# Kernel tuning notes

Hardware: AMD Instinct MI355X
Metric: run time of the kernel (lower is better)

## Reference

```python
import jax, jax.numpy as jnp
import numpy as np

B, C, H, W = 4, 128, 128, 128
_PARAM_IDS = ["1", "2", "4", "5", "7", "8", "9", "10", "12", "13", "15", "16"]


def setup_inputs() -> dict:
    key = jax.random.key(0)
    ks = jax.random.split(key, 2 + 2 * len(_PARAM_IDS))
    scale = 1.0 / np.sqrt(C).astype(np.float32)
    inp = {
        "x": jax.random.normal(ks[0], (B, C, H, W), jnp.float32),
        "y": jax.random.uniform(ks[1], (B, C, H, W), jnp.float32),  # edge gate in [0,1)
    }
    for i, n in enumerate(_PARAM_IDS):
        inp[f"w{n}"] = jax.random.normal(ks[2 + 2 * i], (C, C), jnp.float32) * scale
        inp[f"b{n}"] = jax.random.normal(ks[3 + 2 * i], (C,), jnp.float32) * scale
    return inp


def pw(t, w, b):
    # kernel-size-1 Conv1d: t [B,C,M] -> [B,C,M]
    return jnp.einsum('oc,bcm->bom', w, t) + b[None, :, None]


def gated_scan(seq_x, seq_y, wa, ba, wb, bb, relu_first):
    # seq_x, seq_y: [L, B, C, M]; recurrence h_k = relu(conv_a(x_k) + conv_b(h_{k-1}) * y_{k-1})
    first = jax.nn.relu(seq_x[0]) if relu_first else seq_x[0]

    def step(prev, inp):
        xi, yp = inp
        h = jax.nn.relu(pw(xi, wa, ba) + pw(prev, wb, bb) * yp)
        return h, h

    _, outs = jax.lax.scan(step, first, (seq_x[1:], seq_y[:-1]))
    return jnp.concatenate([first[None], outs], axis=0)


def reference(x, y, w1, b1, w2, b2, w4, b4, w5, b5, w7, b7, w8, b8,
              w9, b9, w10, b10, w12, b12, w13, b13, w15, b15, w16, b16):
    rows_x = jnp.transpose(x, (2, 0, 1, 3))   # [H,B,C,W]
    rows_y = jnp.transpose(y, (2, 0, 1, 3))   # [H,B,C,W]
    y_cols = jnp.transpose(y, (3, 0, 1, 2))   # [W,B,C,H]

    # south scan over height (row 0 untouched, no relu on it)
    hs_rows = gated_scan(rows_x, rows_y, w1, b1, w2, b2, relu_first=False)
    hs_cols = jnp.transpose(hs_rows, (3, 1, 2, 0))  # [W,B,C,H]
    # south-east / south-west scans over width (boundary column gets relu)
    hse = gated_scan(hs_cols, y_cols, w4, b4, w5, b5, relu_first=True)
    hsw = gated_scan(hs_cols[::-1], y_cols[::-1], w7, b7, w8, b8, relu_first=True)[::-1]

    # north scan over height (reversed; boundary row gets relu)
    hn_rows = gated_scan(rows_x[::-1], rows_y[::-1], w9, b9, w10, b10, relu_first=True)[::-1]
    hn_cols = jnp.transpose(hn_rows, (3, 1, 2, 0))  # [W,B,C,H]
    hne = gated_scan(hn_cols, y_cols, w12, b12, w13, b13, relu_first=True)
    hnw = gated_scan(hn_cols[::-1], y_cols[::-1], w15, b15, w16, b16, relu_first=True)[::-1]

    out_cols = hse + hsw + hne + hnw  # [W,B,C,H]
    return jnp.transpose(out_cols, (1, 2, 3, 0))  # [B,C,H,W]
```

## Files before the change

### kernel.cpp

```cpp
#include <hip/hip_runtime.h>

typedef unsigned int uint;
typedef unsigned short ushort;
typedef __attribute__((ext_vector_type(8))) short short8;
typedef __attribute__((ext_vector_type(4))) float f32x4;

#define NPOS 16384
#define PLANE 2097152
#define XR_OFF 0
#define GR_OFF 32768
#define HP_OFF 65536
#define OR_OFF 81920
#define LDS_PH1 81920
#define LDS_PH2 114688

__device__ __forceinline__ uint fbits(float a) { return __builtin_bit_cast(uint, a); }
__device__ __forceinline__ uint rnehi(float a) {
  const uint u = fbits(a);
  return (u + 0x7FFFu + ((u >> 16) & 1u)) & 0xFFFF0000u;
}
__device__ __forceinline__ float fhi(float a) { return __builtin_bit_cast(float, rnehi(a)); }
__device__ __forceinline__ uint packhi(float a, float b) { return (rnehi(a) >> 16) | rnehi(b); }
__device__ __forceinline__ uint packtr(float a, float b) {
  return (fbits(a) >> 16) | (fbits(b) & 0xFFFF0000u);
}
__device__ __forceinline__ float b2f(uint h16) { return __builtin_bit_cast(float, h16 << 16); }

__device__ __forceinline__ f32x4 MF(short8 a, short8 b, f32x4 c) {
  return __builtin_amdgcn_mfma_f32_16x16x32_bf16(a, b, c, 0, 0, 0);
}
__device__ __forceinline__ void fill16(const void* g, char* l) {
  __builtin_amdgcn_global_load_lds((const __attribute__((address_space(1))) void*)g,
                                   (__attribute__((address_space(3))) void*)l, 16, 0, 0);
}
__device__ __forceinline__ void split8(float4 v0, float4 v1, short8& hi, short8& lo) {
  union { short8 s; uint u[4]; } H, L;
  H.u[0] = packhi(v0.x, v0.y); H.u[1] = packhi(v0.z, v0.w);
  H.u[2] = packhi(v1.x, v1.y); H.u[3] = packhi(v1.z, v1.w);
  L.u[0] = packtr(v0.x - fhi(v0.x), v0.y - fhi(v0.y));
  L.u[1] = packtr(v0.z - fhi(v0.z), v0.w - fhi(v0.w));
  L.u[2] = packtr(v1.x - fhi(v1.x), v1.y - fhi(v1.y));
  L.u[3] = packtr(v1.z - fhi(v1.z), v1.w - fhi(v1.w));
  hi = H.s; lo = L.s;
}

#define BAR() asm volatile("s_waitcnt lgkmcnt(0)\n\ts_barrier" ::: "memory")

__global__ __launch_bounds__(256) void k_transpose_x(const float* __restrict__ x,
                                                     ushort* __restrict__ xhi,
                                                     ushort* __restrict__ xlo) {
  __shared__ float tile[128][129];
  const int b = blockIdx.x >> 7, h = blockIdx.x & 127;
  const int t = threadIdx.x, half = t >> 7, lane = t & 127;
  const float* src = x + (size_t)b * PLANE + (size_t)h * 128;
  for (int c0 = 0; c0 < 128; c0 += 2) {
    const int c = c0 + half;
    tile[c][lane] = src[(size_t)c * NPOS + lane];
  }
  __syncthreads();
  const int wq = t >> 6, cp = t & 63;
  for (int w0 = 0; w0 < 128; w0 += 4) {
    const int w = w0 + wq;
    const float v0 = tile[2 * cp][w], v1 = tile[2 * cp + 1][w];
    const size_t e = ((size_t)(b * 128 + w) * 128 + h) * 128 + 2 * cp;
    *(uint*)(xhi + e) = packhi(v0, v1);
    *(uint*)(xlo + e) = packtr(v0 - fhi(v0), v1 - fhi(v1));
  }
}

__global__ __launch_bounds__(256) void k_transpose_y(const float* __restrict__ y,
                                                     float* __restrict__ yt1,
                                                     float* __restrict__ yt2) {
  __shared__ float tile[128][129];
  const int b = blockIdx.x >> 7, h = blockIdx.x & 127;
  const int t = threadIdx.x, half = t >> 7, lane = t & 127;
  const float* src = y + (size_t)b * PLANE + (size_t)h * 128;
  for (int c0 = 0; c0 < 128; c0 += 2) {
    const int c = c0 + half;
    tile[c][lane] = src[(size_t)c * NPOS + lane];
  }
  __syncthreads();
  float* d1 = yt1 + (size_t)b * PLANE + (size_t)h * 128;
  float* d2 = yt2 + ((size_t)(b * 128 + h)) * NPOS;
  for (int w0 = 0; w0 < 128; w0 += 2) {
    const int w = w0 + half;
    const float v = tile[lane][w];
    d1[(size_t)w * NPOS + lane] = v;
    d2[(size_t)w * 128 + lane] = v;
  }
}

template <bool RELU0, bool REV, bool ACCUM, bool OUT16>
__device__ __forceinline__ void scan16(
    char* lds,
    const ushort* __restrict__ xhi, const ushort* __restrict__ xlo, size_t in_base,
    const float* __restrict__ gate, size_t gate_base,
    float* __restrict__ outf, ushort* __restrict__ outhi, ushort* __restrict__ outlo,
    size_t out_base, int out_ps, int out_ls,
    const float* __restrict__ Wa, const float* __restrict__ Ba,
    const float* __restrict__ Wb, const float* __restrict__ Bb) {
  const int t = threadIdx.x;
  const int wv = t >> 6, l = t & 63;
  const int line = l & 15, g4 = l >> 4;

  short8 wah[2][4], wal[2][4], wbh[2][4], wbl[2][4];
#pragma unroll
  for (int tt = 0; tt < 2; ++tt)
#pragma unroll
    for (int kt = 0; kt < 4; ++kt) {
      const int row = 32 * wv + 16 * tt + line;
      const int kc = 32 * kt + 8 * g4;
      split8(*(const float4*)(Wa + row * 128 + kc), *(const float4*)(Wa + row * 128 + kc + 4),
             wah[tt][kt], wal[tt][kt]);
      split8(*(const float4*)(Wb + row * 128 + kc), *(const float4*)(Wb + row * 128 + kc + 4),
             wbh[tt][kt], wbl[tt][kt]);
    }
  f32x4 baf[2], bbf[2];
#pragma unroll
  for (int tt = 0; tt < 2; ++tt) {
    baf[tt] = *(const f32x4*)(Ba + 32 * wv + 16 * tt + 4 * g4);
    bbf[tt] = *(const f32x4*)(Bb + 32 * wv + 16 * tt + 4 * g4);
  }

  auto P = [](int p) -> int { return REV ? 127 - p : p; };

  const int sp = wv >> 1;
  const ushort* xsrc = sp ? xlo : xhi;
  const int lf = l & 15;

  auto fillX = [&](int p, int slot) {
#pragma unroll
    for (int f = 0; f < 2; ++f) {
      const int kg = 2 * (wv & 1) + f;
      const int cc = 4 * kg + (l >> 4);
      fill16(xsrc + in_base + (size_t)lf * NPOS + (size_t)p * 128 + 8 * cc,
             lds + XR_OFF + slot * 8192 + sp * 4096 + kg * 1024 + l * 16);
    }
  };
  auto fillG = [&](int p, int slot) {
#pragma unroll
    for (int f = 0; f < 2; ++f)
      fill16(gate + gate_base + (size_t)lf * NPOS + (size_t)p * 128 + 32 * wv + 16 * f + 4 * (l >> 4),
             lds + GR_OFF + slot * 8192 + wv * 2048 + f * 1024 + l * 16);
  };
  auto fillO = [&](int p, int slot) {
#pragma unroll
    for (int f = 0; f < 2; ++f)
      fill16(outf + out_base + (size_t)p * out_ps + (size_t)lf * out_ls + 32 * wv + 16 * f + 4 * (l >> 4),
             lds + OR_OFF + slot * 8192 + wv * 2048 + f * 1024 + l * 16);
  };

#pragma unroll
  for (int p = 0; p < 4; ++p) {
    fillX(P(p), p);
    if (p < 3) fillG(P(p), p);
    if (ACCUM) fillO(P(p), p);
  }
  asm volatile("s_waitcnt vmcnt(0) lgkmcnt(0)\n\ts_barrier" ::: "memory");

  {
    char* Hwr = lds + HP_OFF;
#pragma unroll
    for (int tt = 0; tt < 2; ++tt) {
      const int cw = 4 * wv + 2 * tt + (g4 >> 1);
      const int boff = (cw * 16 + line) * 16 + 8 * (g4 & 1);
      const uint2 xh = *(const uint2*)(lds + XR_OFF + boff);
      const uint2 xl = *(const uint2*)(lds + XR_OFF + 4096 + boff);
      float4 f;
      f.x = b2f(xh.x & 0xFFFFu) + b2f(xl.x & 0xFFFFu);
      f.y = b2f(xh.x >> 16) + b2f(xl.x >> 16);
      f.z = b2f(xh.y & 0xFFFFu) + b2f(xl.y & 0xFFFFu);
      f.w = b2f(xh.y >> 16) + b2f(xl.y >> 16);
      if (RELU0) {
        f.x = fmaxf(f.x, 0.f); f.y = fmaxf(f.y, 0.f);
        f.z = fmaxf(f.z, 0.f); f.w = fmaxf(f.w, 0.f);
      }
      uint2 hw, lw;
      hw.x = packhi(f.x, f.y); hw.y = packhi(f.z, f.w);
      lw.x = packtr(f.x - fhi(f.x), f.y - fhi(f.y));
      lw.y = packtr(f.z - fhi(f.z), f.w - fhi(f.w));
      *(uint2*)(Hwr + boff) = hw;
      *(uint2*)(Hwr + 4096 + boff) = lw;
      const int ci0 = 32 * wv + 16 * tt + 4 * g4;
      const size_t oe = out_base + (size_t)P(0) * out_ps + (size_t)line * out_ls + ci0;
      if (OUT16) {
        *(uint2*)(outhi + oe) = hw;
        *(uint2*)(outlo + oe) = lw;
      } else {
        float4 o = f;
        if (ACCUM) {
          const f32x4 ov = *(const f32x4*)(lds + OR_OFF + wv * 2048 + tt * 1024 + l * 16);
          o.x += ov[0]; o.y += ov[1]; o.z += ov[2]; o.w += ov[3];
        }
        *(float4*)(outf + oe) = o;
      }
    }
  }
  BAR();

#pragma unroll 1
  for (int s = 1; s < 128; ++s) {
    if (s <= 124) {
      fillX(P(s + 3), (s + 3) & 3);
      fillG(P(s + 2), (s + 2) & 3);
      if (ACCUM) fillO(P(s + 3), (s + 3) & 3);
    }

    f32x4 aF0 = baf[0], aF1 = baf[1], aR0 = bbf[0], aR1 = bbf[1];
    const char* H = lds + HP_OFF + ((s - 1) & 1) * 8192;
    const char* X = lds + XR_OFF + (s & 3) * 8192;
    __builtin_amdgcn_s_setprio(1);
#pragma unroll
    for (int kt = 0; kt < 4; ++kt) {
      const short8 hh = *(const short8*)(H + kt * 1024 + l * 16);
      const short8 hl = *(const short8*)(H + 4096 + kt * 1024 + l * 16);
      const short8 xh = *(const short8*)(X + kt * 1024 + l * 16);
      const short8 xl = *(const short8*)(X + 4096 + kt * 1024 + l * 16);
      aR0 = MF(wbh[0][kt], hh, aR0);
      aR1 = MF(wbh[1][kt], hh, aR1);
      aF0 = MF(wah[0][kt], xh, aF0);
      aF1 = MF(wah[1][kt], xh, aF1);
      aR0 = MF(wbh[0][kt], hl, aR0);
      aR1 = MF(wbh[1][kt], hl, aR1);
      aF0 = MF(wah[0][kt], xl, aF0);
      aF1 = MF(wah[1][kt], xl, aF1);
      aR0 = MF(wbl[0][kt], hh, aR0);
      aR1 = MF(wbl[1][kt], hh, aR1);
      aF0 = MF(wal[0][kt], xh, aF0);
      aF1 = MF(wal[1][kt], xh, aF1);
    }
    __builtin_amdgcn_s_setprio(0);

    const char* Grd = lds + GR_OFF + ((s - 1) & 3) * 8192 + wv * 2048;
    const char* Ord = lds + OR_OFF + (s & 3) * 8192 + wv * 2048;
    char* Hwr = lds + HP_OFF + (s & 1) * 8192;
    const f32x4 aR[2] = {aR0, aR1}, aF[2] = {aF0, aF1};
#pragma unroll
    for (int tt = 0; tt < 2; ++tt) {
      const f32x4 g = *(const f32x4*)(Grd + tt * 1024 + l * 16);
      float4 h;
      h.x = fmaxf(fmaf(aR[tt][0], g[0], aF[tt][0]), 0.f);
      h.y = fmaxf(fmaf(aR[tt][1], g[1], aF[tt][1]), 0.f);
      h.z = fmaxf(fmaf(aR[tt][2], g[2], aF[tt][2]), 0.f);
      h.w = fmaxf(fmaf(aR[tt][3], g[3], aF[tt][3]), 0.f);
      uint2 hw, lw;
      hw.x = packhi(h.x, h.y); hw.y = packhi(h.z, h.w);
      lw.x = packtr(h.x - fhi(h.x), h.y - fhi(h.y));
      lw.y = packtr(h.z - fhi(h.z), h.w - fhi(h.w));
      const int cw = 4 * wv + 2 * tt + (g4 >> 1);
      const int boff = (cw * 16 + line) * 16 + 8 * (g4 & 1);
      *(uint2*)(Hwr + boff) = hw;
      *(uint2*)(Hwr + 4096 + boff) = lw;
      const int ci0 = 32 * wv + 16 * tt + 4 * g4;
      const size_t oe = out_base + (size_t)P(s) * out_ps + (size_t)line * out_ls + ci0;
      if (OUT16) {
        *(uint2*)(outhi + oe) = hw;
        *(uint2*)(outlo + oe) = lw;
      } else {
        float4 o = h;
        if (ACCUM) {
          const f32x4 ov = *(const f32x4*)(Ord + tt * 1024 + l * 16);
          o.x += ov[0]; o.y += ov[1]; o.z += ov[2]; o.w += ov[3];
        }
        *(float4*)(outf + oe) = o;
      }
    }
    if constexpr (ACCUM)
      asm volatile("s_waitcnt vmcnt(16)" ::: "memory");
    else if constexpr (OUT16)
      asm volatile("s_waitcnt vmcnt(18)" ::: "memory");
    else
      asm volatile("s_waitcnt vmcnt(12)" ::: "memory");
    BAR();
  }
}

__global__ __launch_bounds__(256, 1) void k_scan_ph1(
    const ushort* __restrict__ xhi, const ushort* __restrict__ xlo,
    const float* __restrict__ yt1,
    ushort* __restrict__ hs_hi, ushort* __restrict__ hs_lo,
    ushort* __restrict__ hn_hi, ushort* __restrict__ hn_lo,
    const float* w1, const float* b1, const float* w2, const float* b2,
    const float* w9, const float* b9, const float* w10, const float* b10) {
  __shared__ __align__(16) char lds[LDS_PH1];
  const int id = blockIdx.x;
  const int scan = id >> 5, b = (id >> 3) & 3, wg = id & 7;
  const size_t in_base = ((size_t)(b * 128 + wg * 16)) * NPOS;
  const size_t out_base = (size_t)b * PLANE + (size_t)(wg * 16) * 128;
  if (scan == 0)
    scan16<false, false, false, true>(lds, xhi, xlo, in_base, yt1, in_base,
                                      nullptr, hs_hi, hs_lo, out_base, NPOS, 128,
                                      w1, b1, w2, b2);
  else
    scan16<true, true, false, true>(lds, xhi, xlo, in_base, yt1, in_base,
                                    nullptr, hn_hi, hn_lo, out_base, NPOS, 128,
                                    w9, b9, w10, b10);
}

__global__ __launch_bounds__(256, 1) void k_scan_ph2(
    const ushort* __restrict__ hs_hi, const ushort* __restrict__ hs_lo,
    const ushort* __restrict__ hn_hi, const ushort* __restrict__ hn_lo,
    const float* __restrict__ yt2, float* __restrict__ outA, float* __restrict__ outB,
    const float* w4, const float* b4, const float* w5, const float* b5,
    const float* w7, const float* b7, const float* w8, const float* b8,
    const float* w12, const float* b12, const float* w13, const float* b13,
    const float* w15, const float* b15, const float* w16, const float* b16) {
  __shared__ __align__(16) char lds[LDS_PH2];
  const int id = blockIdx.x;
  const int grp = id >> 5, b = (id >> 3) & 3, hg = id & 7;
  const size_t base = ((size_t)(b * 128 + hg * 16)) * NPOS;
  const ushort* ihi = grp ? hn_hi : hs_hi;
  const ushort* ilo = grp ? hn_lo : hs_lo;
  float* o = grp ? outB : outA;
  const float* wa1 = grp ? w12 : w4; const float* ba1 = grp ? b12 : b4;
  const float* wb1 = grp ? w13 : w5; const float* bb1 = grp ? b13 : b5;
  const float* wa2 = grp ? w15 : w7; const float* ba2 = grp ? b15 : b7;
  const float* wb2 = grp ? w16 : w8; const float* bb2 = grp ? b16 : b8;
  scan16<true, false, false, false>(lds, ihi, ilo, base, yt2, base,
                                    o, nullptr, nullptr, base, 128, NPOS,
                                    wa1, ba1, wb1, bb1);
  asm volatile("s_waitcnt vmcnt(0) lgkmcnt(0)\n\ts_barrier" ::: "memory");
  scan16<true, true, true, false>(lds, ihi, ilo, base, yt2, base,
                                  o, nullptr, nullptr, base, 128, NPOS,
                                  wa2, ba2, wb2, bb2);
}

__global__ __launch_bounds__(256) void k_final(const float* __restrict__ outA,
                                               const float* __restrict__ outB,
                                               float* __restrict__ out) {
  __shared__ float tile[128][129];
  const int b = blockIdx.x >> 7, h = blockIdx.x & 127;
  const int t = threadIdx.x, half = t >> 7, lane = t & 127;
  const float* pa = outA + ((size_t)(b * 128 + h)) * NPOS;
  const float* pb = outB + ((size_t)(b * 128 + h)) * NPOS;
  for (int w0 = 0; w0 < 128; w0 += 2) {
    const int w = w0 + half;
    tile[w][lane] = pa[(size_t)w * 128 + lane] + pb[(size_t)w * 128 + lane];
  }
  __syncthreads();
  float* dst = out + (size_t)b * PLANE + (size_t)h * 128;
  for (int c0 = 0; c0 < 128; c0 += 2) {
    const int c = c0 + half;
    dst[(size_t)c * NPOS + lane] = tile[lane][c];
  }
}

extern "C" void kernel_launch(void* const* d_in, const int* in_sizes, int n_in,
                              void* d_out, int out_size, void* d_ws, size_t ws_size,
                              hipStream_t stream) {
  const float* x = (const float*)d_in[0];
  const float* y = (const float*)d_in[1];
  const float* w1 = (const float*)d_in[2];  const float* b1 = (const float*)d_in[3];
  const float* w2 = (const float*)d_in[4];  const float* b2 = (const float*)d_in[5];
  const float* w4 = (const float*)d_in[6];  const float* b4 = (const float*)d_in[7];
  const float* w5 = (const float*)d_in[8];  const float* b5 = (const float*)d_in[9];
  const float* w7 = (const float*)d_in[10]; const float* b7 = (const float*)d_in[11];
  const float* w8 = (const float*)d_in[12]; const float* b8 = (const float*)d_in[13];
  const float* w9 = (const float*)d_in[14]; const float* b9 = (const float*)d_in[15];
  const float* w10 = (const float*)d_in[16]; const float* b10 = (const float*)d_in[17];
  const float* w12 = (const float*)d_in[18]; const float* b12 = (const float*)d_in[19];
  const float* w13 = (const float*)d_in[20]; const float* b13 = (const float*)d_in[21];
  const float* w15 = (const float*)d_in[22]; const float* b15 = (const float*)d_in[23];
  const float* w16 = (const float*)d_in[24]; const float* b16 = (const float*)d_in[25];

  if (ws_size < 167772160) return;
  char* ws = (char*)d_ws;
  ushort* xt_hi = (ushort*)ws;
  ushort* xt_lo = (ushort*)(ws + 16777216);
  float* yt1 = (float*)(ws + 33554432);
  float* yt2 = (float*)(ws + 67108864);
  ushort* hs_hi = (ushort*)(ws + 100663296);
  ushort* hs_lo = (ushort*)(ws + 117440512);
  ushort* hn_hi = (ushort*)(ws + 134217728);
  ushort* hn_lo = (ushort*)(ws + 150994944);
  float* outA = (float*)ws;
  float* outB = (float*)(ws + 33554432);

  dim3 blk(256);
  k_transpose_x<<<512, blk, 0, stream>>>(x, xt_hi, xt_lo);
  k_transpose_y<<<512, blk, 0, stream>>>(y, yt1, yt2);
  k_scan_ph1<<<64, blk, 0, stream>>>(xt_hi, xt_lo, yt1, hs_hi, hs_lo, hn_hi, hn_lo,
                                     w1, b1, w2, b2, w9, b9, w10, b10);
  k_scan_ph2<<<64, blk, 0, stream>>>(hs_hi, hs_lo, hn_hi, hn_lo, yt2, outA, outB,
                                     w4, b4, w5, b5, w7, b7, w8, b8,
                                     w12, b12, w13, b13, w15, b15, w16, b16);
  k_final<<<512, blk, 0, stream>>>(outA, outB, (float*)d_out);
}
```

Measured before the change: 430.0 us.

## Split phase-2 scans into four parallel directions accumulating via float atomics

Phase 2 previously ran 64 blocks, each doing two sequential 128-step scans (east then west) and carrying a running output through LDS. Now 128 blocks each run one direction and add their results straight into a single zeroed accumulator with global float atomicAdd. A zeroing kernel is added and the final kernel reads only one buffer. This doubles parallelism on the serial scan and halves its per-block chain length. The cost is atomic traffic (four scalar atomics per float4), an extra zero pass, and a summation order that is no longer deterministic.

```diff
diff --git a/kernel.cpp b/kernel.cpp
--- a/kernel.cpp
+++ b/kernel.cpp
@@ -10,9 +10,7 @@
 #define XR_OFF 0
 #define GR_OFF 32768
 #define HP_OFF 65536
-#define OR_OFF 81920
-#define LDS_PH1 81920
-#define LDS_PH2 114688
+#define LDS_BYTES 81920
 
 __device__ __forceinline__ uint fbits(float a) { return __builtin_bit_cast(uint, a); }
 __device__ __forceinline__ uint rnehi(float a) {
@@ -90,7 +88,13 @@
   }
 }
 
-template <bool RELU0, bool REV, bool ACCUM, bool OUT16>
+__global__ __launch_bounds__(256) void k_zero(float4* __restrict__ p, int n4) {
+  int i = blockIdx.x * 256 + threadIdx.x;
+  const int stride = gridDim.x * 256;
+  for (; i < n4; i += stride) p[i] = make_float4(0.f, 0.f, 0.f, 0.f);
+}
+
+template <bool RELU0, bool REV, bool OUT16>
 __device__ __forceinline__ void scan16(
     char* lds,
     const ushort* __restrict__ xhi, const ushort* __restrict__ xlo, size_t in_base,
@@ -143,18 +147,11 @@
       fill16(gate + gate_base + (size_t)lf * NPOS + (size_t)p * 128 + 32 * wv + 16 * f + 4 * (l >> 4),
              lds + GR_OFF + slot * 8192 + wv * 2048 + f * 1024 + l * 16);
   };
-  auto fillO = [&](int p, int slot) {
-#pragma unroll
-    for (int f = 0; f < 2; ++f)
-      fill16(outf + out_base + (size_t)p * out_ps + (size_t)lf * out_ls + 32 * wv + 16 * f + 4 * (l >> 4),
-             lds + OR_OFF + slot * 8192 + wv * 2048 + f * 1024 + l * 16);
-  };
 
 #pragma unroll
   for (int p = 0; p < 4; ++p) {
     fillX(P(p), p);
     if (p < 3) fillG(P(p), p);
-    if (ACCUM) fillO(P(p), p);
   }
   asm volatile("s_waitcnt vmcnt(0) lgkmcnt(0)\n\ts_barrier" ::: "memory");
 
@@ -187,12 +184,9 @@
         *(uint2*)(outhi + oe) = hw;
         *(uint2*)(outlo + oe) = lw;
       } else {
-        float4 o = f;
-        if (ACCUM) {
-          const f32x4 ov = *(const f32x4*)(lds + OR_OFF + wv * 2048 + tt * 1024 + l * 16);
-          o.x += ov[0]; o.y += ov[1]; o.z += ov[2]; o.w += ov[3];
-        }
-        *(float4*)(outf + oe) = o;
+        float* op = outf + oe;
+        atomicAdd(op + 0, f.x); atomicAdd(op + 1, f.y);
+        atomicAdd(op + 2, f.z); atomicAdd(op + 3, f.w);
       }
     }
   }
@@ -203,7 +197,6 @@
     if (s <= 124) {
       fillX(P(s + 3), (s + 3) & 3);
       fillG(P(s + 2), (s + 2) & 3);
-      if (ACCUM) fillO(P(s + 3), (s + 3) & 3);
     }
 
     f32x4 aF0 = baf[0], aF1 = baf[1], aR0 = bbf[0], aR1 = bbf[1];
@@ -232,7 +225,6 @@
     __builtin_amdgcn_s_setprio(0);
 
     const char* Grd = lds + GR_OFF + ((s - 1) & 3) * 8192 + wv * 2048;
-    const char* Ord = lds + OR_OFF + (s & 3) * 8192 + wv * 2048;
     char* Hwr = lds + HP_OFF + (s & 1) * 8192;
     const f32x4 aR[2] = {aR0, aR1}, aF[2] = {aF0, aF1};
 #pragma unroll
@@ -257,20 +249,15 @@
         *(uint2*)(outhi + oe) = hw;
         *(uint2*)(outlo + oe) = lw;
       } else {
-        float4 o = h;
-        if (ACCUM) {
-          const f32x4 ov = *(const f32x4*)(Ord + tt * 1024 + l * 16);
-          o.x += ov[0]; o.y += ov[1]; o.z += ov[2]; o.w += ov[3];
-        }
-        *(float4*)(outf + oe) = o;
+        float* op = outf + oe;
+        atomicAdd(op + 0, h.x); atomicAdd(op + 1, h.y);
+        atomicAdd(op + 2, h.z); atomicAdd(op + 3, h.w);
       }
     }
-    if constexpr (ACCUM)
-      asm volatile("s_waitcnt vmcnt(16)" ::: "memory");
-    else if constexpr (OUT16)
+    if constexpr (OUT16)
       asm volatile("s_waitcnt vmcnt(18)" ::: "memory");
     else
-      asm volatile("s_waitcnt vmcnt(12)" ::: "memory");
+      asm volatile("s_waitcnt vmcnt(28)" ::: "memory");
     BAR();
   }
 }
@@ -282,60 +269,56 @@
     ushort* __restrict__ hn_hi, ushort* __restrict__ hn_lo,
     const float* w1, const float* b1, const float* w2, const float* b2,
     const float* w9, const float* b9, const float* w10, const float* b10) {
-  __shared__ __align__(16) char lds[LDS_PH1];
+  __shared__ __align__(16) char lds[LDS_BYTES];
   const int id = blockIdx.x;
   const int scan = id >> 5, b = (id >> 3) & 3, wg = id & 7;
   const size_t in_base = ((size_t)(b * 128 + wg * 16)) * NPOS;
   const size_t out_base = (size_t)b * PLANE + (size_t)(wg * 16) * 128;
   if (scan == 0)
-    scan16<false, false, false, true>(lds, xhi, xlo, in_base, yt1, in_base,
-                                      nullptr, hs_hi, hs_lo, out_base, NPOS, 128,
-                                      w1, b1, w2, b2);
+    scan16<false, false, true>(lds, xhi, xlo, in_base, yt1, in_base,
+                               nullptr, hs_hi, hs_lo, out_base, NPOS, 128,
+                               w1, b1, w2, b2);
   else
-    scan16<true, true, false, true>(lds, xhi, xlo, in_base, yt1, in_base,
-                                    nullptr, hn_hi, hn_lo, out_base, NPOS, 128,
-                                    w9, b9, w10, b10);
+    scan16<true, true, true>(lds, xhi, xlo, in_base, yt1, in_base,
+                             nullptr, hn_hi, hn_lo, out_base, NPOS, 128,
+                             w9, b9, w10, b10);
 }
 
 __global__ __launch_bounds__(256, 1) void k_scan_ph2(
     const ushort* __restrict__ hs_hi, const ushort* __restrict__ hs_lo,
     const ushort* __restrict__ hn_hi, const ushort* __restrict__ hn_lo,
-    const float* __restrict__ yt2, float* __restrict__ outA, float* __restrict__ outB,
+    const float* __restrict__ yt2, float* __restrict__ acc,
     const float* w4, const float* b4, const float* w5, const float* b5,
     const float* w7, const float* b7, const float* w8, const float* b8,
     const float* w12, const float* b12, const float* w13, const float* b13,
     const float* w15, const float* b15, const float* w16, const float* b16) {
-  __shared__ __align__(16) char lds[LDS_PH2];
+  __shared__ __align__(16) char lds[LDS_BYTES];
   const int id = blockIdx.x;
-  const int grp = id >> 5, b = (id >> 3) & 3, hg = id & 7;
+  const int dir = id >> 5, b = (id >> 3) & 3, hg = id & 7;
   const size_t base = ((size_t)(b * 128 + hg * 16)) * NPOS;
-  const ushort* ihi = grp ? hn_hi : hs_hi;
-  const ushort* ilo = grp ? hn_lo : hs_lo;
-  float* o = grp ? outB : outA;
-  const float* wa1 = grp ? w12 : w4; const float* ba1 = grp ? b12 : b4;
-  const float* wb1 = grp ? w13 : w5; const float* bb1 = grp ? b13 : b5;
-  const float* wa2 = grp ? w15 : w7; const float* ba2 = grp ? b15 : b7;
-  const float* wb2 = grp ? w16 : w8; const float* bb2 = grp ? b16 : b8;
-  scan16<true, false, false, false>(lds, ihi, ilo, base, yt2, base,
-                                    o, nullptr, nullptr, base, 128, NPOS,
-                                    wa1, ba1, wb1, bb1);
-  asm volatile("s_waitcnt vmcnt(0) lgkmcnt(0)\n\ts_barrier" ::: "memory");
-  scan16<true, true, true, false>(lds, ihi, ilo, base, yt2, base,
-                                  o, nullptr, nullptr, base, 128, NPOS,
-                                  wa2, ba2, wb2, bb2);
-}
-
-__global__ __launch_bounds__(256) void k_final(const float* __restrict__ outA,
-                                               const float* __restrict__ outB,
+  const ushort* ihi = (dir >> 1) ? hn_hi : hs_hi;
+  const ushort* ilo = (dir >> 1) ? hn_lo : hs_lo;
+  const float* wa = (dir == 0) ? w4 : (dir == 1) ? w7 : (dir == 2) ? w12 : w15;
+  const float* ba = (dir == 0) ? b4 : (dir == 1) ? b7 : (dir == 2) ? b12 : b15;
+  const float* wb = (dir == 0) ? w5 : (dir == 1) ? w8 : (dir == 2) ? w13 : w16;
+  const float* bb = (dir == 0) ? b5 : (dir == 1) ? b8 : (dir == 2) ? b13 : b16;
+  if (dir & 1)
+    scan16<true, true, false>(lds, ihi, ilo, base, yt2, base,
+                              acc, nullptr, nullptr, base, 128, NPOS, wa, ba, wb, bb);
+  else
+    scan16<true, false, false>(lds, ihi, ilo, base, yt2, base,
+                               acc, nullptr, nullptr, base, 128, NPOS, wa, ba, wb, bb);
+}
+
+__global__ __launch_bounds__(256) void k_final(const float* __restrict__ acc,
                                                float* __restrict__ out) {
   __shared__ float tile[128][129];
   const int b = blockIdx.x >> 7, h = blockIdx.x & 127;
   const int t = threadIdx.x, half = t >> 7, lane = t & 127;
-  const float* pa = outA + ((size_t)(b * 128 + h)) * NPOS;
-  const float* pb = outB + ((size_t)(b * 128 + h)) * NPOS;
+  const float* pa = acc + ((size_t)(b * 128 + h)) * NPOS;
   for (int w0 = 0; w0 < 128; w0 += 2) {
     const int w = w0 + half;
-    tile[w][lane] = pa[(size_t)w * 128 + lane] + pb[(size_t)w * 128 + lane];
+    tile[w][lane] = pa[(size_t)w * 128 + lane];
   }
   __syncthreads();
   float* dst = out + (size_t)b * PLANE + (size_t)h * 128;
@@ -373,16 +356,16 @@
   ushort* hs_lo = (ushort*)(ws + 117440512);
   ushort* hn_hi = (ushort*)(ws + 134217728);
   ushort* hn_lo = (ushort*)(ws + 150994944);
-  float* outA = (float*)ws;
-  float* outB = (float*)(ws + 33554432);
+  float* acc = (float*)ws;
 
   dim3 blk(256);
   k_transpose_x<<<512, blk, 0, stream>>>(x, xt_hi, xt_lo);
   k_transpose_y<<<512, blk, 0, stream>>>(y, yt1, yt2);
   k_scan_ph1<<<64, blk, 0, stream>>>(xt_hi, xt_lo, yt1, hs_hi, hs_lo, hn_hi, hn_lo,
                                      w1, b1, w2, b2, w9, b9, w10, b10);
-  k_scan_ph2<<<64, blk, 0, stream>>>(hs_hi, hs_lo, hn_hi, hn_lo, yt2, outA, outB,
-                                     w4, b4, w5, b5, w7, b7, w8, b8,
-                                     w12, b12, w13, b13, w15, b15, w16, b16);
-  k_final<<<512, blk, 0, stream>>>(outA, outB, (float*)d_out);
-}
+  k_zero<<<2048, blk, 0, stream>>>((float4*)acc, 2097152);
+  k_scan_ph2<<<128, blk, 0, stream>>>(hs_hi, hs_lo, hn_hi, hn_lo, yt2, acc,
+                                      w4, b4, w5, b5, w7, b7, w8, b8,
+                                      w12, b12, w13, b13, w15, b15, w16, b16);
+  k_final<<<512, blk, 0, stream>>>(acc, (float*)d_out);
+}
```

Result: slower. 593.9 us (+38.1%).

## Prefetch scan inputs into registers instead of async LDS staging

Applied to the files above, without the earlier changes.

Replaces the async global-to-LDS fill pipeline for x, gate and accumulator tiles with direct register loads that are double-buffered through compile-time slots, shrinking LDS to the hidden-state ping-pong buffer only. The step loop is unrolled by two so the slot indices are static. It also splits each MFMA chain into two independent accumulators per output to shorten the dependency chain. The aim is to take LDS traffic and hand-tuned vmcnt waits off the serial recurrence path, at the cost of higher register pressure and global loads that may not be fully hidden before use.

```diff
diff --git a/kernel.cpp b/kernel.cpp
--- a/kernel.cpp
+++ b/kernel.cpp
@@ -7,12 +7,9 @@
 
 #define NPOS 16384
 #define PLANE 2097152
-#define XR_OFF 0
-#define GR_OFF 32768
-#define HP_OFF 65536
-#define OR_OFF 81920
-#define LDS_PH1 81920
-#define LDS_PH2 114688
+#define LDS_BYTES 16384
+
+template <int N> struct IC { static constexpr int value = N; };
 
 __device__ __forceinline__ uint fbits(float a) { return __builtin_bit_cast(uint, a); }
 __device__ __forceinline__ uint rnehi(float a) {
@@ -28,10 +25,6 @@
 
 __device__ __forceinline__ f32x4 MF(short8 a, short8 b, f32x4 c) {
   return __builtin_amdgcn_mfma_f32_16x16x32_bf16(a, b, c, 0, 0, 0);
-}
-__device__ __forceinline__ void fill16(const void* g, char* l) {
-  __builtin_amdgcn_global_load_lds((const __attribute__((address_space(1))) void*)g,
-                                   (__attribute__((address_space(3))) void*)l, 16, 0, 0);
 }
 __device__ __forceinline__ void split8(float4 v0, float4 v1, short8& hi, short8& lo) {
   union { short8 s; uint u[4]; } H, L;
@@ -124,48 +117,43 @@
 
   auto P = [](int p) -> int { return REV ? 127 - p : p; };
 
-  const int sp = wv >> 1;
-  const ushort* xsrc = sp ? xlo : xhi;
-  const int lf = l & 15;
-
-  auto fillX = [&](int p, int slot) {
-#pragma unroll
-    for (int f = 0; f < 2; ++f) {
-      const int kg = 2 * (wv & 1) + f;
-      const int cc = 4 * kg + (l >> 4);
-      fill16(xsrc + in_base + (size_t)lf * NPOS + (size_t)p * 128 + 8 * cc,
-             lds + XR_OFF + slot * 8192 + sp * 4096 + kg * 1024 + l * 16);
+  const size_t xoff = in_base + (size_t)line * NPOS + 8 * g4;
+  const size_t goff = gate_base + (size_t)line * NPOS + 32 * wv + 4 * g4;
+  const size_t ooff = out_base + (size_t)line * out_ls + 32 * wv + 4 * g4;
+
+  short8 XH[2][4], XL[2][4];
+  f32x4 GV[2][2], OV[2][2];
+
+  auto loadX = [&](auto SL, int pos) {
+    constexpr int sl = decltype(SL)::value;
+    const size_t e = xoff + (size_t)pos * 128;
+#pragma unroll
+    for (int kt = 0; kt < 4; ++kt) {
+      XH[sl][kt] = *(const short8*)(xhi + e + 32 * kt);
+      XL[sl][kt] = *(const short8*)(xlo + e + 32 * kt);
     }
   };
-  auto fillG = [&](int p, int slot) {
-#pragma unroll
-    for (int f = 0; f < 2; ++f)
-      fill16(gate + gate_base + (size_t)lf * NPOS + (size_t)p * 128 + 32 * wv + 16 * f + 4 * (l >> 4),
-             lds + GR_OFF + slot * 8192 + wv * 2048 + f * 1024 + l * 16);
+  auto loadG = [&](auto SL, int gpos) {
+    constexpr int sl = decltype(SL)::value;
+    const size_t e = goff + (size_t)gpos * 128;
+    GV[sl][0] = *(const f32x4*)(gate + e);
+    GV[sl][1] = *(const f32x4*)(gate + e + 16);
   };
-  auto fillO = [&](int p, int slot) {
-#pragma unroll
-    for (int f = 0; f < 2; ++f)
-      fill16(outf + out_base + (size_t)p * out_ps + (size_t)lf * out_ls + 32 * wv + 16 * f + 4 * (l >> 4),
-             lds + OR_OFF + slot * 8192 + wv * 2048 + f * 1024 + l * 16);
+  auto loadO = [&](auto SL, int pos) {
+    constexpr int sl = decltype(SL)::value;
+    const size_t e = ooff + (size_t)pos * out_ps;
+    OV[sl][0] = *(const f32x4*)(outf + e);
+    OV[sl][1] = *(const f32x4*)(outf + e + 16);
   };
 
-#pragma unroll
-  for (int p = 0; p < 4; ++p) {
-    fillX(P(p), p);
-    if (p < 3) fillG(P(p), p);
-    if (ACCUM) fillO(P(p), p);
-  }
-  asm volatile("s_waitcnt vmcnt(0) lgkmcnt(0)\n\ts_barrier" ::: "memory");
-
   {
-    char* Hwr = lds + HP_OFF;
+    char* Hwr = lds;
 #pragma unroll
     for (int tt = 0; tt < 2; ++tt) {
-      const int cw = 4 * wv + 2 * tt + (g4 >> 1);
-      const int boff = (cw * 16 + line) * 16 + 8 * (g4 & 1);
-      const uint2 xh = *(const uint2*)(lds + XR_OFF + boff);
-      const uint2 xl = *(const uint2*)(lds + XR_OFF + 4096 + boff);
+      const int ci0 = 32 * wv + 16 * tt + 4 * g4;
+      const size_t xe = in_base + (size_t)line * NPOS + (size_t)P(0) * 128 + ci0;
+      const uint2 xh = *(const uint2*)(xhi + xe);
+      const uint2 xl = *(const uint2*)(xlo + xe);
       float4 f;
       f.x = b2f(xh.x & 0xFFFFu) + b2f(xl.x & 0xFFFFu);
       f.y = b2f(xh.x >> 16) + b2f(xl.x >> 16);
@@ -179,70 +167,68 @@
       hw.x = packhi(f.x, f.y); hw.y = packhi(f.z, f.w);
       lw.x = packtr(f.x - fhi(f.x), f.y - fhi(f.y));
       lw.y = packtr(f.z - fhi(f.z), f.w - fhi(f.w));
+      const int cw = 4 * wv + 2 * tt + (g4 >> 1);
+      const int boff = (cw * 16 + line) * 16 + 8 * (g4 & 1);
       *(uint2*)(Hwr + boff) = hw;
       *(uint2*)(Hwr + 4096 + boff) = lw;
-      const int ci0 = 32 * wv + 16 * tt + 4 * g4;
-      const size_t oe = out_base + (size_t)P(0) * out_ps + (size_t)line * out_ls + ci0;
+      const size_t oe = ooff + (size_t)P(0) * out_ps + 16 * tt;
       if (OUT16) {
         *(uint2*)(outhi + oe) = hw;
         *(uint2*)(outlo + oe) = lw;
       } else {
         float4 o = f;
         if (ACCUM) {
-          const f32x4 ov = *(const f32x4*)(lds + OR_OFF + wv * 2048 + tt * 1024 + l * 16);
-          o.x += ov[0]; o.y += ov[1]; o.z += ov[2]; o.w += ov[3];
+          const float4 ov = *(const float4*)(outf + oe);
+          o.x += ov.x; o.y += ov.y; o.z += ov.z; o.w += ov.w;
         }
         *(float4*)(outf + oe) = o;
       }
     }
   }
+  loadX(IC<1>{}, P(1)); loadG(IC<1>{}, P(0));
+  loadX(IC<0>{}, P(2)); loadG(IC<0>{}, P(1));
+  if constexpr (ACCUM) { loadO(IC<1>{}, P(1)); loadO(IC<0>{}, P(2)); }
   BAR();
 
-#pragma unroll 1
-  for (int s = 1; s < 128; ++s) {
-    if (s <= 124) {
-      fillX(P(s + 3), (s + 3) & 3);
-      fillG(P(s + 2), (s + 2) & 3);
-      if (ACCUM) fillO(P(s + 3), (s + 3) & 3);
-    }
-
-    f32x4 aF0 = baf[0], aF1 = baf[1], aR0 = bbf[0], aR1 = bbf[1];
-    const char* H = lds + HP_OFF + ((s - 1) & 1) * 8192;
-    const char* X = lds + XR_OFF + (s & 3) * 8192;
+  auto body = [&](auto SL, int s) {
+    constexpr int sl = decltype(SL)::value;
+    const char* Hrd = lds + (sl ^ 1) * 8192;
+    char* Hwr = lds + sl * 8192;
+    const f32x4 z = {0.f, 0.f, 0.f, 0.f};
+    f32x4 aFa[2] = {baf[0], baf[1]}, aFb[2] = {z, z};
+    f32x4 aRa[2] = {bbf[0], bbf[1]}, aRb[2] = {z, z};
     __builtin_amdgcn_s_setprio(1);
-#pragma unroll
-    for (int kt = 0; kt < 4; ++kt) {
-      const short8 hh = *(const short8*)(H + kt * 1024 + l * 16);
-      const short8 hl = *(const short8*)(H + 4096 + kt * 1024 + l * 16);
-      const short8 xh = *(const short8*)(X + kt * 1024 + l * 16);
-      const short8 xl = *(const short8*)(X + 4096 + kt * 1024 + l * 16);
-      aR0 = MF(wbh[0][kt], hh, aR0);
-      aR1 = MF(wbh[1][kt], hh, aR1);
-      aF0 = MF(wah[0][kt], xh, aF0);
-      aF1 = MF(wah[1][kt], xh, aF1);
-      aR0 = MF(wbh[0][kt], hl, aR0);
-      aR1 = MF(wbh[1][kt], hl, aR1);
-      aF0 = MF(wah[0][kt], xl, aF0);
-      aF1 = MF(wah[1][kt], xl, aF1);
-      aR0 = MF(wbl[0][kt], hh, aR0);
-      aR1 = MF(wbl[1][kt], hh, aR1);
-      aF0 = MF(wal[0][kt], xh, aF0);
-      aF1 = MF(wal[1][kt], xh, aF1);
-    }
+#define KT(kt, AF, AR)                                                    \
+    {                                                                     \
+      const short8 hh = *(const short8*)(Hrd + kt * 1024 + l * 16);       \
+      const short8 hl = *(const short8*)(Hrd + 4096 + kt * 1024 + l * 16);\
+      AF[0] = MF(wah[0][kt], XH[sl][kt], AF[0]);                          \
+      AF[1] = MF(wah[1][kt], XH[sl][kt], AF[1]);                          \
+      AF[0] = MF(wah[0][kt], XL[sl][kt], AF[0]);                          \
+      AF[1] = MF(wah[1][kt], XL[sl][kt], AF[1]);                          \
+      AF[0] = MF(wal[0][kt], XH[sl][kt], AF[0]);                          \
+      AF[1] = MF(wal[1][kt], XH[sl][kt], AF[1]);                          \
+      AR[0] = MF(wbh[0][kt], hh, AR[0]);                                  \
+      AR[1] = MF(wbh[1][kt], hh, AR[1]);                                  \
+      AR[0] = MF(wbh[0][kt], hl, AR[0]);                                  \
+      AR[1] = MF(wbh[1][kt], hl, AR[1]);                                  \
+      AR[0] = MF(wbl[0][kt], hh, AR[0]);                                  \
+      AR[1] = MF(wbl[1][kt], hh, AR[1]);                                  \
+    }
+    KT(0, aFa, aRa) KT(1, aFb, aRb) KT(2, aFa, aRa) KT(3, aFb, aRb)
+#undef KT
     __builtin_amdgcn_s_setprio(0);
 
-    const char* Grd = lds + GR_OFF + ((s - 1) & 3) * 8192 + wv * 2048;
-    const char* Ord = lds + OR_OFF + (s & 3) * 8192 + wv * 2048;
-    char* Hwr = lds + HP_OFF + (s & 1) * 8192;
-    const f32x4 aR[2] = {aR0, aR1}, aF[2] = {aF0, aF1};
+    const f32x4 aFv[2] = {aFa[0] + aFb[0], aFa[1] + aFb[1]};
+    const f32x4 aRv[2] = {aRa[0] + aRb[0], aRa[1] + aRb[1]};
 #pragma unroll
     for (int tt = 0; tt < 2; ++tt) {
-      const f32x4 g = *(const f32x4*)(Grd + tt * 1024 + l * 16);
+      const f32x4 g = GV[sl][tt];
       float4 h;
-      h.x = fmaxf(fmaf(aR[tt][0], g[0], aF[tt][0]), 0.f);
-      h.y = fmaxf(fmaf(aR[tt][1], g[1], aF[tt][1]), 0.f);
-      h.z = fmaxf(fmaf(aR[tt][2], g[2], aF[tt][2]), 0.f);
-      h.w = fmaxf(fmaf(aR[tt][3], g[3], aF[tt][3]), 0.f);
+      h.x = fmaxf(fmaf(aRv[tt][0], g[0], aFv[tt][0]), 0.f);
+      h.y = fmaxf(fmaf(aRv[tt][1], g[1], aFv[tt][1]), 0.f);
+      h.z = fmaxf(fmaf(aRv[tt][2], g[2], aFv[tt][2]), 0.f);
+      h.w = fmaxf(fmaf(aRv[tt][3], g[3], aFv[tt][3]), 0.f);
       uint2 hw, lw;
       hw.x = packhi(h.x, h.y); hw.y = packhi(h.z, h.w);
       lw.x = packtr(h.x - fhi(h.x), h.y - fhi(h.y));
@@ -251,28 +237,33 @@
       const int boff = (cw * 16 + line) * 16 + 8 * (g4 & 1);
       *(uint2*)(Hwr + boff) = hw;
       *(uint2*)(Hwr + 4096 + boff) = lw;
-      const int ci0 = 32 * wv + 16 * tt + 4 * g4;
-      const size_t oe = out_base + (size_t)P(s) * out_ps + (size_t)line * out_ls + ci0;
+      const size_t oe = ooff + (size_t)P(s) * out_ps + 16 * tt;
       if (OUT16) {
         *(uint2*)(outhi + oe) = hw;
         *(uint2*)(outlo + oe) = lw;
       } else {
         float4 o = h;
         if (ACCUM) {
-          const f32x4 ov = *(const f32x4*)(Ord + tt * 1024 + l * 16);
+          const f32x4 ov = OV[sl][tt];
           o.x += ov[0]; o.y += ov[1]; o.z += ov[2]; o.w += ov[3];
         }
         *(float4*)(outf + oe) = o;
       }
     }
-    if constexpr (ACCUM)
-      asm volatile("s_waitcnt vmcnt(16)" ::: "memory");
-    else if constexpr (OUT16)
-      asm volatile("s_waitcnt vmcnt(18)" ::: "memory");
-    else
-      asm volatile("s_waitcnt vmcnt(12)" ::: "memory");
+    const int pn = (s + 2 < 128) ? (s + 2) : 127;
+    const int gn = (s + 1 < 128) ? (s + 1) : 127;
+    loadX(SL, P(pn));
+    loadG(SL, P(gn));
+    if constexpr (ACCUM) loadO(SL, P(pn));
     BAR();
-  }
+  };
+
+#pragma unroll 1
+  for (int s = 1; s <= 125; s += 2) {
+    body(IC<1>{}, s);
+    body(IC<0>{}, s + 1);
+  }
+  body(IC<1>{}, 127);
 }
 
 __global__ __launch_bounds__(256, 1) void k_scan_ph1(
@@ -282,7 +273,7 @@
     ushort* __restrict__ hn_hi, ushort* __restrict__ hn_lo,
     const float* w1, const float* b1, const float* w2, const float* b2,
     const float* w9, const float* b9, const float* w10, const float* b10) {
-  __shared__ __align__(16) char lds[LDS_PH1];
+  __shared__ __align__(16) char lds[LDS_BYTES];
   const int id = blockIdx.x;
   const int scan = id >> 5, b = (id >> 3) & 3, wg = id & 7;
   const size_t in_base = ((size_t)(b * 128 + wg * 16)) * NPOS;
@@ -305,7 +296,7 @@
     const float* w7, const float* b7, const float* w8, const float* b8,
     const float* w12, const float* b12, const float* w13, const float* b13,
     const float* w15, const float* b15, const float* w16, const float* b16) {
-  __shared__ __align__(16) char lds[LDS_PH2];
+  __shared__ __align__(16) char lds[LDS_BYTES];
   const int id = blockIdx.x;
   const int grp = id >> 5, b = (id >> 3) & 3, hg = id & 7;
   const size_t base = ((size_t)(b * 128 + hg * 16)) * NPOS;
```

Result: slower. 581.2 us (+35.2%).

## Run forward and reverse width scans concurrently with midpoint flag handoff

Applied to the files above, without the earlier changes.

Phase 2 previously ran the east and west width scans back to back inside one block. Now 128 blocks run them at the same time, one direction per block. At the midpoint each block publishes a flag and waits for its partner's flag, then accumulates the partner's already written second half of the output. This roughly halves the serial recurrence length per block. The cost is a cross-block spin-wait that relies on all 128 blocks being co-resident, plus a flag array kept in the output buffer and zeroed by an extra launch.

```diff
diff --git a/kernel.cpp b/kernel.cpp
--- a/kernel.cpp
+++ b/kernel.cpp
@@ -90,7 +90,9 @@
   }
 }
 
-template <bool RELU0, bool REV, bool ACCUM, bool OUT16>
+__global__ void k_zeroflags(int* __restrict__ f) { f[threadIdx.x] = 0; }
+
+template <bool RELU0, bool REV, bool MID, bool OUT16>
 __device__ __forceinline__ void scan16(
     char* lds,
     const ushort* __restrict__ xhi, const ushort* __restrict__ xlo, size_t in_base,
@@ -98,7 +100,8 @@
     float* __restrict__ outf, ushort* __restrict__ outhi, ushort* __restrict__ outlo,
     size_t out_base, int out_ps, int out_ls,
     const float* __restrict__ Wa, const float* __restrict__ Ba,
-    const float* __restrict__ Wb, const float* __restrict__ Bb) {
+    const float* __restrict__ Wb, const float* __restrict__ Bb,
+    int* myflag, int* pflag) {
   const int t = threadIdx.x;
   const int wv = t >> 6, l = t & 63;
   const int line = l & 15, g4 = l >> 4;
@@ -154,7 +157,6 @@
   for (int p = 0; p < 4; ++p) {
     fillX(P(p), p);
     if (p < 3) fillG(P(p), p);
-    if (ACCUM) fillO(P(p), p);
   }
   asm volatile("s_waitcnt vmcnt(0) lgkmcnt(0)\n\ts_barrier" ::: "memory");
 
@@ -187,12 +189,7 @@
         *(uint2*)(outhi + oe) = hw;
         *(uint2*)(outlo + oe) = lw;
       } else {
-        float4 o = f;
-        if (ACCUM) {
-          const f32x4 ov = *(const f32x4*)(lds + OR_OFF + wv * 2048 + tt * 1024 + l * 16);
-          o.x += ov[0]; o.y += ov[1]; o.z += ov[2]; o.w += ov[3];
-        }
-        *(float4*)(outf + oe) = o;
+        *(float4*)(outf + oe) = f;
       }
     }
   }
@@ -200,11 +197,20 @@
 
 #pragma unroll 1
   for (int s = 1; s < 128; ++s) {
+    if (MID && s == 64) {
+      while (__hip_atomic_load(pflag, __ATOMIC_ACQUIRE, __HIP_MEMORY_SCOPE_AGENT) == 0)
+        __builtin_amdgcn_s_sleep(2);
+      fillO(P(64), 0);
+      fillO(P(65), 1);
+      fillO(P(66), 2);
+    }
     if (s <= 124) {
       fillX(P(s + 3), (s + 3) & 3);
       fillG(P(s + 2), (s + 2) & 3);
-      if (ACCUM) fillO(P(s + 3), (s + 3) & 3);
-    }
+      if (MID && s >= 64) fillO(P(s + 3), (s + 3) & 3);
+    }
+    if (MID && s == 64)
+      asm volatile("s_waitcnt vmcnt(0)" ::: "memory");
 
     f32x4 aF0 = baf[0], aF1 = baf[1], aR0 = bbf[0], aR1 = bbf[1];
     const char* H = lds + HP_OFF + ((s - 1) & 1) * 8192;
@@ -258,20 +264,26 @@
         *(uint2*)(outlo + oe) = lw;
       } else {
         float4 o = h;
-        if (ACCUM) {
+        if (MID && s >= 64) {
           const f32x4 ov = *(const f32x4*)(Ord + tt * 1024 + l * 16);
           o.x += ov[0]; o.y += ov[1]; o.z += ov[2]; o.w += ov[3];
         }
         *(float4*)(outf + oe) = o;
       }
     }
-    if constexpr (ACCUM)
+    if constexpr (MID)
       asm volatile("s_waitcnt vmcnt(16)" ::: "memory");
     else if constexpr (OUT16)
       asm volatile("s_waitcnt vmcnt(18)" ::: "memory");
     else
       asm volatile("s_waitcnt vmcnt(12)" ::: "memory");
     BAR();
+    if (MID && s == 63) {
+      asm volatile("s_waitcnt vmcnt(0)" ::: "memory");
+      __builtin_amdgcn_s_barrier();
+      if (threadIdx.x == 0)
+        __hip_atomic_store(myflag, 1, __ATOMIC_RELEASE, __HIP_MEMORY_SCOPE_AGENT);
+    }
   }
 }
 
@@ -290,39 +302,48 @@
   if (scan == 0)
     scan16<false, false, false, true>(lds, xhi, xlo, in_base, yt1, in_base,
                                       nullptr, hs_hi, hs_lo, out_base, NPOS, 128,
-                                      w1, b1, w2, b2);
+                                      w1, b1, w2, b2, nullptr, nullptr);
   else
     scan16<true, true, false, true>(lds, xhi, xlo, in_base, yt1, in_base,
                                     nullptr, hn_hi, hn_lo, out_base, NPOS, 128,
-                                    w9, b9, w10, b10);
+                                    w9, b9, w10, b10, nullptr, nullptr);
 }
 
 __global__ __launch_bounds__(256, 1) void k_scan_ph2(
     const ushort* __restrict__ hs_hi, const ushort* __restrict__ hs_lo,
     const ushort* __restrict__ hn_hi, const ushort* __restrict__ hn_lo,
     const float* __restrict__ yt2, float* __restrict__ outA, float* __restrict__ outB,
+    int* __restrict__ flags,
     const float* w4, const float* b4, const float* w5, const float* b5,
     const float* w7, const float* b7, const float* w8, const float* b8,
     const float* w12, const float* b12, const float* w13, const float* b13,
     const float* w15, const float* b15, const float* w16, const float* b16) {
   __shared__ __align__(16) char lds[LDS_PH2];
   const int id = blockIdx.x;
-  const int grp = id >> 5, b = (id >> 3) & 3, hg = id & 7;
+  const int rev = id >> 6, rest = id & 63;
+  const int grp = rest >> 5, b = (rest >> 3) & 3, hg = rest & 7;
   const size_t base = ((size_t)(b * 128 + hg * 16)) * NPOS;
   const ushort* ihi = grp ? hn_hi : hs_hi;
   const ushort* ilo = grp ? hn_lo : hs_lo;
   float* o = grp ? outB : outA;
-  const float* wa1 = grp ? w12 : w4; const float* ba1 = grp ? b12 : b4;
-  const float* wb1 = grp ? w13 : w5; const float* bb1 = grp ? b13 : b5;
-  const float* wa2 = grp ? w15 : w7; const float* ba2 = grp ? b15 : b7;
-  const float* wb2 = grp ? w16 : w8; const float* bb2 = grp ? b16 : b8;
-  scan16<true, false, false, false>(lds, ihi, ilo, base, yt2, base,
+  int* myf = flags + rest * 2 + rev;
+  int* pf = flags + rest * 2 + (rev ^ 1);
+  const float* wa; const float* ba; const float* wb; const float* bb;
+  if (grp == 0) {
+    wa = rev ? w7 : w4;  ba = rev ? b7 : b4;
+    wb = rev ? w8 : w5;  bb = rev ? b8 : b5;
+  } else {
+    wa = rev ? w15 : w12; ba = rev ? b15 : b12;
+    wb = rev ? w16 : w13; bb = rev ? b16 : b13;
+  }
+  if (rev)
+    scan16<true, true, true, false>(lds, ihi, ilo, base, yt2, base,
                                     o, nullptr, nullptr, base, 128, NPOS,
-                                    wa1, ba1, wb1, bb1);
-  asm volatile("s_waitcnt vmcnt(0) lgkmcnt(0)\n\ts_barrier" ::: "memory");
-  scan16<true, true, true, false>(lds, ihi, ilo, base, yt2, base,
-                                  o, nullptr, nullptr, base, 128, NPOS,
-                                  wa2, ba2, wb2, bb2);
+                                    wa, ba, wb, bb, myf, pf);
+  else
+    scan16<true, false, true, false>(lds, ihi, ilo, base, yt2, base,
+                                     o, nullptr, nullptr, base, 128, NPOS,
+                                     wa, ba, wb, bb, myf, pf);
 }
 
 __global__ __launch_bounds__(256) void k_final(const float* __restrict__ outA,
@@ -375,14 +396,16 @@
   ushort* hn_lo = (ushort*)(ws + 150994944);
   float* outA = (float*)ws;
   float* outB = (float*)(ws + 33554432);
+  int* flags = (int*)d_out;
 
   dim3 blk(256);
   k_transpose_x<<<512, blk, 0, stream>>>(x, xt_hi, xt_lo);
   k_transpose_y<<<512, blk, 0, stream>>>(y, yt1, yt2);
+  k_zeroflags<<<1, 128, 0, stream>>>(flags);
   k_scan_ph1<<<64, blk, 0, stream>>>(xt_hi, xt_lo, yt1, hs_hi, hs_lo, hn_hi, hn_lo,
                                      w1, b1, w2, b2, w9, b9, w10, b10);
-  k_scan_ph2<<<64, blk, 0, stream>>>(hs_hi, hs_lo, hn_hi, hn_lo, yt2, outA, outB,
-                                     w4, b4, w5, b5, w7, b7, w8, b8,
-                                     w12, b12, w13, b13, w15, b15, w16, b16);
+  k_scan_ph2<<<128, blk, 0, stream>>>(hs_hi, hs_lo, hn_hi, hn_lo, yt2, outA, outB, flags,
+                                      w4, b4, w5, b5, w7, b7, w8, b8,
+                                      w12, b12, w13, b13, w15, b15, w16, b16);
   k_final<<<512, blk, 0, stream>>>(outA, outB, (float*)d_out);
 }
```

Result: faster. 387.2 us (-10.0%).
